# Optimization experiments

Measured on AMD Instinct MI355X. Metric: run time of the kernel, lower is better.

The kernel has to match this reference:

```python
import jax, jax.numpy as jnp
import numpy as np

WH, WW = 8, 8
NUM_HEADS = 8
DIM = 256
MLP_HIDDEN = 1024
EPS = 1e-5


def _rel_pos_index(wh, ww):
    ch, cw = np.meshgrid(np.arange(wh), np.arange(ww), indexing='ij')
    flat = np.stack([ch.ravel(), cw.ravel()])            # (2, N)
    rel = flat[:, :, None] - flat[:, None, :]            # (2, N, N)
    rel = rel.transpose(1, 2, 0).copy()                  # (N, N, 2)
    rel[:, :, 0] += wh - 1
    rel[:, :, 1] += ww - 1
    rel[:, :, 0] *= 2 * ww - 1
    return jnp.asarray(rel.sum(-1))                      # (N, N) int

REL_IDX = _rel_pos_index(WH, WW)


def _layernorm(x, g, b):
    mu = x.mean(-1, keepdims=True)
    var = ((x - mu) ** 2).mean(-1, keepdims=True)
    return (x - mu) * jax.lax.rsqrt(var + EPS) * g + b


def _window_partition(x):
    B, H, W, C = x.shape
    x = x.reshape(B, H // WH, WH, W // WW, WW, C)
    return x.transpose(0, 1, 3, 2, 4, 5).reshape(-1, WH * WW, C)


def _window_reverse(w, B, H, W):
    C = w.shape[-1]
    x = w.reshape(B, H // WH, W // WW, WH, WW, C)
    return x.transpose(0, 1, 3, 2, 4, 5).reshape(B, H, W, C)


def _window_attn(qx, kvx, qw, qb, kvw, kvb, bias_table, pw, pb):
    # qx/kvx: [Bw, N, C]; weights stored as [in, out] (torch Linear transposed)
    Bw, N, C = qx.shape
    hd = C // NUM_HEADS
    scale = hd ** -0.5
    q = (qx @ qw + qb).reshape(Bw, N, NUM_HEADS, hd).transpose(0, 2, 1, 3) * scale
    kv = (kvx @ kvw + kvb).reshape(Bw, N, 2, NUM_HEADS, hd)
    k = kv[:, :, 0].transpose(0, 2, 1, 3)
    v = kv[:, :, 1].transpose(0, 2, 1, 3)
    attn = jnp.einsum('bhnd,bhmd->bhnm', q, k)
    bias = bias_table[REL_IDX.reshape(-1)].reshape(N, N, NUM_HEADS).transpose(2, 0, 1)
    attn = jax.nn.softmax(attn + bias[None], axis=-1)
    out = jnp.einsum('bhnm,bhmd->bhnd', attn, v).transpose(0, 2, 1, 3).reshape(Bw, N, C)
    return out @ pw + pb


def setup_inputs() -> dict:
    key = jax.random.key(0)
    ks = jax.random.split(key, 16)
    B, H, W, C = 4, 160, 160, DIM
    nW = (H // WH) * (W // WW)
    N = WH * WW
    n_bias = (2 * WH - 1) * (2 * WW - 1)  # 225
    s = 0.02
    return {
        'x': jax.random.normal(ks[0], (B, H, W, C), jnp.float32),
        'enc_feat': jax.random.normal(ks[1], (B, H, W, C), jnp.float32),
        'mask_matrix': jnp.zeros((nW, N, N), jnp.float32),
        'norm1_g': jnp.ones((C,), jnp.float32),
        'norm1_b': jnp.zeros((C,), jnp.float32),
        'q1_w': jax.random.normal(ks[2], (C, C), jnp.float32) * s,
        'q1_b': jnp.zeros((C,), jnp.float32),
        'kv1_w': jax.random.normal(ks[3], (C, 2 * C), jnp.float32) * s,
        'kv1_b': jnp.zeros((2 * C,), jnp.float32),
        'bias1': jax.random.normal(ks[4], (n_bias, NUM_HEADS), jnp.float32) * s,
        'proj1_w': jax.random.normal(ks[5], (C, C), jnp.float32) * s,
        'proj1_b': jnp.zeros((C,), jnp.float32),
        'q2_w': jax.random.normal(ks[6], (C, C), jnp.float32) * s,
        'q2_b': jnp.zeros((C,), jnp.float32),
        'kv2_w': jax.random.normal(ks[7], (C, 2 * C), jnp.float32) * s,
        'kv2_b': jnp.zeros((2 * C,), jnp.float32),
        'bias2': jax.random.normal(ks[8], (n_bias, NUM_HEADS), jnp.float32) * s,
        'proj2_w': jax.random.normal(ks[9], (C, C), jnp.float32) * s,
        'proj2_b': jnp.zeros((C,), jnp.float32),
        'norm2_g': jnp.ones((C,), jnp.float32),
        'norm2_b': jnp.zeros((C,), jnp.float32),
        'fc1_w': jax.random.normal(ks[10], (C, MLP_HIDDEN), jnp.float32) * s,
        'fc1_b': jnp.zeros((MLP_HIDDEN,), jnp.float32),
        'fc2_w': jax.random.normal(ks[11], (MLP_HIDDEN, C), jnp.float32) * s,
        'fc2_b': jnp.zeros((C,), jnp.float32),
    }


def reference(x, enc_feat, mask_matrix, norm1_g, norm1_b, q1_w, q1_b, kv1_w, kv1_b,
              bias1, proj1_w, proj1_b, q2_w, q2_b, kv2_w, kv2_b, bias2, proj2_w,
              proj2_b, norm2_g, norm2_b, fc1_w, fc1_b, fc2_w, fc2_b):
    # NOTE: the source forward never passes mask_matrix into attention; faithful here.
    B, H, W, C = x.shape
    shortcut = x
    xn = _layernorm(x, norm1_g, norm1_b)
    xw = _window_partition(xn)              # [B*nW, N, C]
    ew = _window_partition(enc_feat)        # [B*nW, N, C]
    # windowed self-attention with relative position bias
    xw = _window_attn(xw, xw, q1_w, q1_b, kv1_w, kv1_b, bias1, proj1_w, proj1_b)
    # windowed cross-attention to encoder features
    xw = _window_attn(xw, ew, q2_w, q2_b, kv2_w, kv2_b, bias2, proj2_w, proj2_b)
    x = shortcut + _window_reverse(xw, B, H, W)
    h = _layernorm(x, norm2_g, norm2_b)
    h = jax.nn.gelu(h @ fc1_w + fc1_b, approximate=False) @ fc2_w + fc2_b
    return x + h
```

## Files before the change

### kernel.cpp

```cpp
#include <hip/hip_runtime.h>

typedef __attribute__((ext_vector_type(4))) float f32x4;
typedef __attribute__((ext_vector_type(8))) short bf16x8;
typedef __attribute__((ext_vector_type(8))) unsigned short ushort8;
typedef unsigned short u16;
typedef unsigned int u32;

#define LDS_AS(p) ((__attribute__((address_space(3))) void*)(p))
#define GLB_AS(p) ((const __attribute__((address_space(1))) void*)(p))

__device__ __forceinline__ u16 f2b(float f) {
    u32 u = __builtin_bit_cast(u32, f);
    u32 r = (u + 0x7fffu + ((u >> 16) & 1u)) >> 16;
    return (u16)r;
}
__device__ __forceinline__ float b2f(u16 u) {
    return __builtin_bit_cast(float, (u32)u << 16);
}

struct PrepAll {
    const float* src[8];
    u16* dst[8];
    int K[8];
    int N[8];
    float S[8];
};

__global__ __launch_bounds__(256) void prep_w(PrepAll p) {
    const int wi = blockIdx.y;
    const int K = p.K[wi], N = p.N[wi];
    for (int e = blockIdx.x * 256 + threadIdx.x; e < K * N; e += gridDim.x * 256) {
        const int k = e / N, n = e % N;
        p.dst[wi][n * K + k] = f2b(p.src[wi][e] * p.S[wi]);
    }
}

__global__ __launch_bounds__(256) void prep_bias(const float* __restrict__ t1,
                                                 const float* __restrict__ t2,
                                                 float* __restrict__ Bm) {
    const int hh = blockIdx.x;
    const int s = hh >> 3, h = hh & 7;
    const float* tab = s ? t2 : t1;
    const int j = threadIdx.x & 63;
    for (int i = threadIdx.x >> 6; i < 64; i += 4) {
        const int idx = ((i >> 3) - (j >> 3) + 7) * 15 + ((i & 7) - (j & 7) + 7);
        Bm[(long)hh * 4096 + i * 64 + j] = tab[idx * 8 + h];
    }
}

__global__ __launch_bounds__(256) void prep_bcat(const float* __restrict__ q1b,
                                                 const float* __restrict__ q2b,
                                                 float qs, float* __restrict__ q1bs,
                                                 float* __restrict__ q2bs) {
    const int g = threadIdx.x;
    q1bs[g] = qs * q1b[g];
    q2bs[g] = qs * q2b[g];
}

__global__ __launch_bounds__(256) void cast_bf(const float* __restrict__ in,
                                               u16* __restrict__ out, long n8) {
    for (long i = (long)blockIdx.x * 256 + threadIdx.x; i < n8; i += (long)gridDim.x * 256) {
        const float4 a = *(const float4*)(in + i * 8);
        const float4 b = *(const float4*)(in + i * 8 + 4);
        ushort8 o;
        o[0] = f2b(a.x); o[1] = f2b(a.y); o[2] = f2b(a.z); o[3] = f2b(a.w);
        o[4] = f2b(b.x); o[5] = f2b(b.y); o[6] = f2b(b.z); o[7] = f2b(b.w);
        *(ushort8*)(out + i * 8) = o;
    }
}

__global__ __launch_bounds__(256) void ln256(const float* __restrict__ x,
                                             const float* __restrict__ g,
                                             const float* __restrict__ b,
                                             u16* __restrict__ out) {
    const int lane = threadIdx.x & 63;
    const int c = lane * 4;
    const float4 gv = *(const float4*)(g + c);
    const float4 bv = *(const float4*)(b + c);
#pragma unroll
    for (int it = 0; it < 8; ++it) {
        const long row = (long)blockIdx.x * 32 + it * 4 + (threadIdx.x >> 6);
        const float4 v = *(const float4*)(x + row * 256 + c);
        float s = v.x + v.y + v.z + v.w;
        float s2 = v.x * v.x + v.y * v.y + v.z * v.z + v.w * v.w;
#pragma unroll
        for (int off = 32; off > 0; off >>= 1) {
            s += __shfl_xor(s, off);
            s2 += __shfl_xor(s2, off);
        }
        const float mu = s * (1.f / 256.f);
        const float rr = rsqrtf(s2 * (1.f / 256.f) - mu * mu + 1e-5f);
        ushort4 o;
        o.x = f2b((v.x - mu) * rr * gv.x + bv.x);
        o.y = f2b((v.y - mu) * rr * gv.y + bv.y);
        o.z = f2b((v.z - mu) * rr * gv.z + bv.z);
        o.w = f2b((v.w - mu) * rr * gv.w + bv.w);
        *(ushort4*)(out + row * 256 + c) = o;
    }
}

__global__ __launch_bounds__(256) void ln_add(const float* __restrict__ x,
                                              const u16* __restrict__ p,
                                              const float* __restrict__ g,
                                              const float* __restrict__ b,
                                              float* __restrict__ out,
                                              u16* __restrict__ xo) {
    const int lane = threadIdx.x & 63;
    const int c = lane * 4;
    const float4 gv = *(const float4*)(g + c);
    const float4 bv = *(const float4*)(b + c);
#pragma unroll
    for (int it = 0; it < 8; ++it) {
        const long row = (long)blockIdx.x * 32 + it * 4 + (threadIdx.x >> 6);
        float4 v = *(const float4*)(x + row * 256 + c);
        const ushort4 pb = *(const ushort4*)(p + row * 256 + c);
        v.x += b2f(pb.x); v.y += b2f(pb.y); v.z += b2f(pb.z); v.w += b2f(pb.w);
        *(float4*)(out + row * 256 + c) = v;
        float s = v.x + v.y + v.z + v.w;
        float s2 = v.x * v.x + v.y * v.y + v.z * v.z + v.w * v.w;
#pragma unroll
        for (int off = 32; off > 0; off >>= 1) {
            s += __shfl_xor(s, off);
            s2 += __shfl_xor(s2, off);
        }
        const float mu = s * (1.f / 256.f);
        const float rr = rsqrtf(s2 * (1.f / 256.f) - mu * mu + 1e-5f);
        ushort4 o;
        o.x = f2b((v.x - mu) * rr * gv.x + bv.x);
        o.y = f2b((v.y - mu) * rr * gv.y + bv.y);
        o.z = f2b((v.z - mu) * rr * gv.z + bv.z);
        o.w = f2b((v.w - mu) * rr * gv.w + bv.w);
        *(ushort4*)(xo + row * 256 + c) = o;
    }
}

template <int SAME>
__global__ __launch_bounds__(512, 1) void attn_f(const u16* __restrict__ xq,
                                                 const u16* __restrict__ xkv,
                                                 const u16* __restrict__ wq,
                                                 const u16* __restrict__ wkv,
                                                 const float* __restrict__ bq,
                                                 const float* __restrict__ bkv,
                                                 const u16* __restrict__ wp,
                                                 const float* __restrict__ bp,
                                                 const float* __restrict__ Bm,
                                                 u16* __restrict__ OUT) {
    __shared__ u16 LDS[57344];
    const int t = threadIdx.x, lane = t & 63, h = t >> 6;
    const int l15 = lane & 15, lg = lane >> 4;

    const int w = blockIdx.x;
    const int b = w / 400, rem = w % 400;
    const int wy = rem / 20, wx = rem % 20;
    const long base_t = (long)b * 25600 + wy * 1280 + wx * 8;
    auto trow = [&](int r) -> long { return base_t + (r >> 3) * 160 + (r & 7); };

#pragma unroll
    for (int j = 0; j < 4; j++) {
        const int row = j * 16 + (t >> 5);
        const int c0 = t & 31, sc = c0 ^ (row & 7);
        __builtin_amdgcn_global_load_lds(GLB_AS(xq + trow(row) * 256 + sc * 8),
                                         LDS_AS(&LDS[(j * 512 + t) * 8]), 16, 0, 0);
    }
    if (!SAME) {
#pragma unroll
        for (int j = 0; j < 4; j++) {
            const int row = j * 16 + (t >> 5);
            const int c0 = t & 31, sc = c0 ^ (row & 7);
            __builtin_amdgcn_global_load_lds(GLB_AS(xkv + trow(row) * 256 + sc * 8),
                                             LDS_AS(&LDS[16384 + (j * 512 + t) * 8]), 16, 0, 0);
        }
    }
    asm volatile("s_waitcnt vmcnt(0)" ::: "memory");
    __builtin_amdgcn_s_barrier();

    constexpr int XKV = SAME ? 0 : 16384;
    const f32x4 zz = (f32x4){0.f, 0.f, 0.f, 0.f};

    f32x4 aQ[4][2], aK[4][2], aV[4][2];
#pragma unroll
    for (int mi = 0; mi < 4; mi++)
#pragma unroll
        for (int n = 0; n < 2; n++) { aQ[mi][n] = zz; aK[mi][n] = zz; aV[mi][n] = zz; }

    const u16* wv = wkv + 256 * 256;

#define QKV_PASS(ACC, W, XB)                                                              \
    do {                                                                                  \
        bf16x8 wf[2][8];                                                                  \
        _Pragma("unroll") for (int n = 0; n < 2; n++)                                     \
            _Pragma("unroll") for (int s = 0; s < 8; s++)                                 \
                wf[n][s] = *(const bf16x8*)((W) + (h * 32 + n * 16 + l15) * 256 + s * 32 + lg * 8); \
        _Pragma("unroll") for (int s = 0; s < 8; s++) {                                   \
            bf16x8 af[4];                                                                 \
            _Pragma("unroll") for (int mi = 0; mi < 4; mi++)                              \
                af[mi] = *(const bf16x8*)&LDS[(XB) + ((mi * 16 + l15) * 32 +              \
                                              ((s * 4 + lg) ^ (l15 & 7))) * 8];           \
            _Pragma("unroll") for (int mi = 0; mi < 4; mi++)                              \
                _Pragma("unroll") for (int n = 0; n < 2; n++)                             \
                    ACC[mi][n] = __builtin_amdgcn_mfma_f32_16x16x32_bf16(af[mi], wf[n][s], ACC[mi][n], 0, 0, 0); \
        }                                                                                 \
    } while (0)

    QKV_PASS(aQ, wq, 0);
    QKV_PASS(aK, wkv, XKV);
    QKV_PASS(aV, wv, XKV);
#undef QKV_PASS
    __builtin_amdgcn_s_barrier();

    float bQ[2], bK[2], bV[2];
#pragma unroll
    for (int n = 0; n < 2; n++) {
        bQ[n] = bq[h * 32 + n * 16 + l15];
        bK[n] = bkv[h * 32 + n * 16 + l15];
        bV[n] = bkv[256 + h * 32 + n * 16 + l15];
    }

    const int S1 = h * 2560;
#pragma unroll
    for (int mi = 0; mi < 4; mi++)
#pragma unroll
        for (int n = 0; n < 2; n++)
#pragma unroll
            for (int r = 0; r < 4; r++)
                LDS[S1 + (mi * 16 + lg * 4 + r) * 40 + n * 16 + l15] = f2b(aQ[mi][n][r] + bQ[n]);
    bf16x8 qf[4];
#pragma unroll
    for (int ti = 0; ti < 4; ti++)
        qf[ti] = *(const bf16x8*)&LDS[S1 + (ti * 16 + l15) * 40 + lg * 8];
#pragma unroll
    for (int mi = 0; mi < 4; mi++)
#pragma unroll
        for (int n = 0; n < 2; n++)
#pragma unroll
            for (int r = 0; r < 4; r++)
                LDS[S1 + (mi * 16 + lg * 4 + r) * 40 + n * 16 + l15] = f2b(aK[mi][n][r] + bK[n]);
    bf16x8 kf[4];
#pragma unroll
    for (int ti = 0; ti < 4; ti++)
        kf[ti] = *(const bf16x8*)&LDS[S1 + (ti * 16 + l15) * 40 + lg * 8];

    f32x4 s4[4][4];
#pragma unroll
    for (int ti = 0; ti < 4; ti++)
#pragma unroll
        for (int tj = 0; tj < 4; tj++)
            s4[ti][tj] = __builtin_amdgcn_mfma_f32_16x16x32_bf16(qf[ti], kf[tj], zz, 0, 0, 0);

#pragma unroll
    for (int mi = 0; mi < 4; mi++)
#pragma unroll
        for (int n = 0; n < 2; n++)
#pragma unroll
            for (int r = 0; r < 4; r++)
                LDS[S1 + (n * 16 + l15) * 72 + mi * 16 + lg * 4 + r] = f2b(aV[mi][n][r] + bV[n]);

    const int PB = 20480 + h * 4608;
    const float* Bh = Bm + h * 4096;
#pragma unroll
    for (int ti = 0; ti < 4; ti++) {
#pragma unroll
        for (int r = 0; r < 4; r++) {
            const int i = ti * 16 + lg * 4 + r;
            float vv[4];
            float m = -1e30f;
#pragma unroll
            for (int tj = 0; tj < 4; tj++) {
                vv[tj] = s4[ti][tj][r] + Bh[i * 64 + tj * 16 + l15];
                m = fmaxf(m, vv[tj]);
            }
#pragma unroll
            for (int off = 1; off < 16; off <<= 1) m = fmaxf(m, __shfl_xor(m, off));
            float sum = 0.f;
#pragma unroll
            for (int tj = 0; tj < 4; tj++) {
                vv[tj] = __expf(vv[tj] - m);
                sum += vv[tj];
            }
#pragma unroll
            for (int off = 1; off < 16; off <<= 1) sum += __shfl_xor(sum, off);
            const float inv = 1.f / sum;
#pragma unroll
            for (int tj = 0; tj < 4; tj++)
                LDS[PB + i * 72 + tj * 16 + l15] = f2b(vv[tj] * inv);
        }
    }

    f32x4 o[4][2];
#pragma unroll
    for (int mi = 0; mi < 4; mi++)
#pragma unroll
        for (int n = 0; n < 2; n++) o[mi][n] = zz;
#pragma unroll
    for (int c = 0; c < 2; c++) {
        bf16x8 vf[2];
#pragma unroll
        for (int n = 0; n < 2; n++)
            vf[n] = *(const bf16x8*)&LDS[S1 + (n * 16 + l15) * 72 + c * 32 + lg * 8];
#pragma unroll
        for (int mi = 0; mi < 4; mi++) {
            bf16x8 pf = *(const bf16x8*)&LDS[PB + (mi * 16 + l15) * 72 + c * 32 + lg * 8];
#pragma unroll
            for (int n = 0; n < 2; n++)
                o[mi][n] = __builtin_amdgcn_mfma_f32_16x16x32_bf16(pf, vf[n], o[mi][n], 0, 0, 0);
        }
    }

    __builtin_amdgcn_s_barrier();
#pragma unroll
    for (int mi = 0; mi < 4; mi++)
#pragma unroll
        for (int n = 0; n < 2; n++)
#pragma unroll
            for (int r = 0; r < 4; r++)
                LDS[(mi * 16 + lg * 4 + r) * 264 + h * 32 + n * 16 + l15] = f2b(o[mi][n][r]);
    __builtin_amdgcn_s_barrier();

    bf16x8 pwf[2][8];
#pragma unroll
    for (int n = 0; n < 2; n++)
#pragma unroll
        for (int s = 0; s < 8; s++)
            pwf[n][s] = *(const bf16x8*)(wp + (h * 32 + n * 16 + l15) * 256 + s * 32 + lg * 8);
    f32x4 pacc[4][2];
#pragma unroll
    for (int mi = 0; mi < 4; mi++)
#pragma unroll
        for (int n = 0; n < 2; n++) pacc[mi][n] = zz;
#pragma unroll
    for (int s = 0; s < 8; s++) {
        bf16x8 paf[4];
#pragma unroll
        for (int mi = 0; mi < 4; mi++)
            paf[mi] = *(const bf16x8*)&LDS[(mi * 16 + l15) * 264 + s * 32 + lg * 8];
#pragma unroll
        for (int mi = 0; mi < 4; mi++)
#pragma unroll
            for (int n = 0; n < 2; n++)
                pacc[mi][n] = __builtin_amdgcn_mfma_f32_16x16x32_bf16(paf[mi], pwf[n][s], pacc[mi][n], 0, 0, 0);
    }
    float pb2[2];
#pragma unroll
    for (int n = 0; n < 2; n++) pb2[n] = bp[h * 32 + n * 16 + l15];
#pragma unroll
    for (int mi = 0; mi < 4; mi++)
#pragma unroll
        for (int n = 0; n < 2; n++)
#pragma unroll
            for (int r = 0; r < 4; r++) {
                const int i = mi * 16 + lg * 4 + r;
                OUT[trow(i) * 256 + h * 32 + n * 16 + l15] = f2b(pacc[mi][n][r] + pb2[n]);
            }
}

__global__ __launch_bounds__(512) void mlpf(const u16* __restrict__ xo,
                                            const u16* __restrict__ w1,
                                            const float* __restrict__ b1,
                                            const u16* __restrict__ w2,
                                            const float* __restrict__ b2,
                                            float* __restrict__ out) {
    __shared__ u16 W[16384];
    __shared__ u16 HS[9216];
    const int t = threadIdx.x, lane = t & 63, h = t >> 6;
    const int l15 = lane & 15, lg = lane >> 4;
    const long r0 = (long)blockIdx.x * 128 + h * 16;
    const f32x4 zz = (f32x4){0.f, 0.f, 0.f, 0.f};

    bf16x8 af[8];
#pragma unroll
    for (int s = 0; s < 8; s++)
        af[s] = *(const bf16x8*)(xo + (r0 + l15) * 256 + s * 32 + lg * 8);

    f32x4 yacc[16];
#pragma unroll
    for (int n = 0; n < 16; n++) yacc[n] = zz;

    const int hsb = h * 1152;

    for (int c = 0; c < 16; ++c) {
        if (c) __builtin_amdgcn_s_barrier();
#pragma unroll
        for (int rnd = 0; rnd < 4; rnd++) {
            const int idx = rnd * 512 + t;
            const int row = idx >> 5, c0 = idx & 31, sc = c0 ^ (row & 7);
            __builtin_amdgcn_global_load_lds(GLB_AS(w1 + (c * 64 + row) * 256 + sc * 8),
                                             LDS_AS(&W[idx * 8]), 16, 0, 0);
        }
        asm volatile("s_waitcnt vmcnt(0)" ::: "memory");
        __builtin_amdgcn_s_barrier();

        float f1bb[4];
#pragma unroll
        for (int n = 0; n < 4; n++) f1bb[n] = b1[c * 64 + n * 16 + l15];

        f32x4 hc[4];
#pragma unroll
        for (int n = 0; n < 4; n++) hc[n] = zz;
#pragma unroll
        for (int s = 0; s < 8; s++) {
            bf16x8 bf[4];
#pragma unroll
            for (int n = 0; n < 4; n++)
                bf[n] = *(const bf16x8*)&W[((n * 16 + l15) * 32 + ((s * 4 + lg) ^ (l15 & 7))) * 8];
#pragma unroll
            for (int n = 0; n < 4; n++)
                hc[n] = __builtin_amdgcn_mfma_f32_16x16x32_bf16(af[s], bf[n], hc[n], 0, 0, 0);
        }
#pragma unroll
        for (int n = 0; n < 4; n++)
#pragma unroll
            for (int r = 0; r < 4; r++) {
                float v = hc[n][r] + f1bb[n];
                v = 0.5f * v * (1.f + erff(v * 0.70710678118f));
                HS[hsb + (lg * 4 + r) * 72 + n * 16 + l15] = f2b(v);
            }
        __builtin_amdgcn_s_barrier();

#pragma unroll
        for (int rnd = 0; rnd < 4; rnd++) {
            const int idx = rnd * 512 + t;
            const int row = idx >> 3, c0 = idx & 7, sc = c0 ^ (row & 7);
            __builtin_amdgcn_global_load_lds(GLB_AS(w2 + row * 1024 + c * 64 + sc * 8),
                                             LDS_AS(&W[idx * 8]), 16, 0, 0);
        }
        asm volatile("s_waitcnt vmcnt(0)" ::: "memory");
        __builtin_amdgcn_s_barrier();

#pragma unroll
        for (int ks = 0; ks < 2; ks++) {
            bf16x8 haf = *(const bf16x8*)&HS[hsb + l15 * 72 + ks * 32 + lg * 8];
            bf16x8 bf2[16];
#pragma unroll
            for (int n = 0; n < 16; n++)
                bf2[n] = *(const bf16x8*)&W[((n * 16 + l15) * 8 + ((ks * 4 + lg) ^ (l15 & 7))) * 8];
#pragma unroll
            for (int n = 0; n < 16; n++)
                yacc[n] = __builtin_amdgcn_mfma_f32_16x16x32_bf16(haf, bf2[n], yacc[n], 0, 0, 0);
        }
    }

    float f2bb[16];
#pragma unroll
    for (int n = 0; n < 16; n++) f2bb[n] = b2[n * 16 + l15];
#pragma unroll
    for (int n = 0; n < 16; n++)
#pragma unroll
        for (int r = 0; r < 4; r++) {
            const long idx = (r0 + lg * 4 + r) * 256 + n * 16 + l15;
            out[idx] = yacc[n][r] + f2bb[n] + out[idx];
        }
}

extern "C" void kernel_launch(void* const* d_in, const int* in_sizes, int n_in,
                              void* d_out, int out_size, void* d_ws, size_t ws_size,
                              hipStream_t stream) {
    const float* x    = (const float*)d_in[0];
    const float* enc  = (const float*)d_in[1];
    const float* n1g  = (const float*)d_in[3];
    const float* n1b  = (const float*)d_in[4];
    const float* q1w  = (const float*)d_in[5];
    const float* q1b  = (const float*)d_in[6];
    const float* kv1w = (const float*)d_in[7];
    const float* kv1b = (const float*)d_in[8];
    const float* bias1 = (const float*)d_in[9];
    const float* p1w  = (const float*)d_in[10];
    const float* p1b  = (const float*)d_in[11];
    const float* q2w  = (const float*)d_in[12];
    const float* q2b  = (const float*)d_in[13];
    const float* kv2w = (const float*)d_in[14];
    const float* kv2b = (const float*)d_in[15];
    const float* bias2 = (const float*)d_in[16];
    const float* p2w  = (const float*)d_in[17];
    const float* p2bi = (const float*)d_in[18];
    const float* n2g  = (const float*)d_in[19];
    const float* n2b  = (const float*)d_in[20];
    const float* f1w  = (const float*)d_in[21];
    const float* f1b  = (const float*)d_in[22];
    const float* f2w  = (const float*)d_in[23];
    const float* f2bias = (const float*)d_in[24];
    float* out = (float*)d_out;

    char* ws = (char*)d_ws;
    size_t off = 0;
    auto alloc = [&](size_t bytes) {
        char* p = ws + off;
        off += (bytes + 255) & ~(size_t)255;
        return p;
    };
    u16* Wt    = (u16*)alloc(1048576 * 2);
    float* Bm  = (float*)alloc(16 * 4096 * 4);
    float* q1s = (float*)alloc(256 * 4);
    float* q2s = (float*)alloc(256 * 4);
    u16* xn    = (u16*)alloc(52428800);
    u16* y1    = (u16*)alloc(52428800);
    u16* pj2   = (u16*)alloc(52428800);
    u16* encb  = (u16*)alloc(52428800);

    u16 *q1t = Wt, *kv1t = Wt + 65536, *p1t = Wt + 196608, *q2t = Wt + 262144,
        *kv2t = Wt + 327680, *p2t = Wt + 458752, *f1t = Wt + 524288, *f2t = Wt + 786432;

    const float qscale = 0.17677669529663687f;

    PrepAll pa;
    pa.src[0] = q1w;  pa.dst[0] = q1t;  pa.K[0] = 256;  pa.N[0] = 256;  pa.S[0] = qscale;
    pa.src[1] = kv1w; pa.dst[1] = kv1t; pa.K[1] = 256;  pa.N[1] = 512;  pa.S[1] = 1.f;
    pa.src[2] = p1w;  pa.dst[2] = p1t;  pa.K[2] = 256;  pa.N[2] = 256;  pa.S[2] = 1.f;
    pa.src[3] = q2w;  pa.dst[3] = q2t;  pa.K[3] = 256;  pa.N[3] = 256;  pa.S[3] = qscale;
    pa.src[4] = kv2w; pa.dst[4] = kv2t; pa.K[4] = 256;  pa.N[4] = 512;  pa.S[4] = 1.f;
    pa.src[5] = p2w;  pa.dst[5] = p2t;  pa.K[5] = 256;  pa.N[5] = 256;  pa.S[5] = 1.f;
    pa.src[6] = f1w;  pa.dst[6] = f1t;  pa.K[6] = 256;  pa.N[6] = 1024; pa.S[6] = 1.f;
    pa.src[7] = f2w;  pa.dst[7] = f2t;  pa.K[7] = 1024; pa.N[7] = 256;  pa.S[7] = 1.f;
    prep_w<<<dim3(128, 8), 256, 0, stream>>>(pa);
    prep_bias<<<dim3(16), 256, 0, stream>>>(bias1, bias2, Bm);
    prep_bcat<<<dim3(1), 256, 0, stream>>>(q1b, q2b, qscale, q1s, q2s);
    cast_bf<<<dim3(2048), 256, 0, stream>>>(enc, encb, 3276800);
    ln256<<<dim3(3200), 256, 0, stream>>>(x, n1g, n1b, xn);

    attn_f<1><<<dim3(1600), 512, 0, stream>>>(xn, xn, q1t, kv1t, q1s, kv1b,
                                              p1t, p1b, Bm, y1);
    attn_f<0><<<dim3(1600), 512, 0, stream>>>(y1, encb, q2t, kv2t, q2s, kv2b,
                                              p2t, p2bi, Bm + 8 * 4096, pj2);

    ln_add<<<dim3(3200), 256, 0, stream>>>(x, pj2, n2g, n2b, out, xn);

    mlpf<<<dim3(800), 512, 0, stream>>>(xn, f1t, f1b, f2t, f2bias, out);
}
```

Before: 820.9 us.

## Shrink LDS and registers to run two blocks per CU in attention and MLP

The attention kernel shrinks its LDS footprint from about 112KB to 76KB. It does this by reusing the per-wave Q/K staging area for the probability tile and splitting the softmax-times-V step into two halves. It also loads weight fragments per k-step instead of all at once, lowering register pressure, and both kernels now request two blocks per CU. The MLP kernel loads the fc1 and fc2 weight chunks together into one larger LDS buffer, removing a barrier and load-wait phase per chunk, and uses an XOR-swizzled hidden buffer instead of padding. The risks are that two blocks per CU may not fit, and that softmax is now computed twice.

```diff
diff --git a/kernel.cpp b/kernel.cpp
--- a/kernel.cpp
+++ b/kernel.cpp
@@ -135,7 +135,7 @@
 }
 
 template <int SAME>
-__global__ __launch_bounds__(512, 1) void attn_f(const u16* __restrict__ xq,
+__global__ __launch_bounds__(512, 2) void attn_f(const u16* __restrict__ xq,
                                                  const u16* __restrict__ xkv,
                                                  const u16* __restrict__ wq,
                                                  const u16* __restrict__ wkv,
@@ -145,7 +145,7 @@
                                                  const float* __restrict__ bp,
                                                  const float* __restrict__ Bm,
                                                  u16* __restrict__ OUT) {
-    __shared__ u16 LDS[57344];
+    __shared__ u16 LDS[38912];
     const int t = threadIdx.x, lane = t & 63, h = t >> 6;
     const int l15 = lane & 15, lg = lane >> 4;
 
@@ -185,21 +185,20 @@
 
     const u16* wv = wkv + 256 * 256;
 
-#define QKV_PASS(ACC, W, XB)                                                              \
-    do {                                                                                  \
-        bf16x8 wf[2][8];                                                                  \
-        _Pragma("unroll") for (int n = 0; n < 2; n++)                                     \
-            _Pragma("unroll") for (int s = 0; s < 8; s++)                                 \
-                wf[n][s] = *(const bf16x8*)((W) + (h * 32 + n * 16 + l15) * 256 + s * 32 + lg * 8); \
-        _Pragma("unroll") for (int s = 0; s < 8; s++) {                                   \
-            bf16x8 af[4];                                                                 \
-            _Pragma("unroll") for (int mi = 0; mi < 4; mi++)                              \
-                af[mi] = *(const bf16x8*)&LDS[(XB) + ((mi * 16 + l15) * 32 +              \
-                                              ((s * 4 + lg) ^ (l15 & 7))) * 8];           \
-            _Pragma("unroll") for (int mi = 0; mi < 4; mi++)                              \
-                _Pragma("unroll") for (int n = 0; n < 2; n++)                             \
-                    ACC[mi][n] = __builtin_amdgcn_mfma_f32_16x16x32_bf16(af[mi], wf[n][s], ACC[mi][n], 0, 0, 0); \
-        }                                                                                 \
+#define QKV_PASS(ACC, W, XB)                                                               \
+    do {                                                                                   \
+        _Pragma("unroll") for (int s = 0; s < 8; s++) {                                    \
+            bf16x8 wf0 = *(const bf16x8*)((W) + (h * 32 + l15) * 256 + s * 32 + lg * 8);   \
+            bf16x8 wf1 = *(const bf16x8*)((W) + (h * 32 + 16 + l15) * 256 + s * 32 + lg * 8); \
+            bf16x8 af[4];                                                                  \
+            _Pragma("unroll") for (int mi = 0; mi < 4; mi++)                               \
+                af[mi] = *(const bf16x8*)&LDS[(XB) + ((mi * 16 + l15) * 32 +               \
+                                              ((s * 4 + lg) ^ (l15 & 7))) * 8];            \
+            _Pragma("unroll") for (int mi = 0; mi < 4; mi++) {                             \
+                ACC[mi][0] = __builtin_amdgcn_mfma_f32_16x16x32_bf16(af[mi], wf0, ACC[mi][0], 0, 0, 0); \
+                ACC[mi][1] = __builtin_amdgcn_mfma_f32_16x16x32_bf16(af[mi], wf1, ACC[mi][1], 0, 0, 0); \
+            }                                                                              \
+        }                                                                                  \
     } while (0)
 
     QKV_PASS(aQ, wq, 0);
@@ -216,29 +215,37 @@
         bV[n] = bkv[256 + h * 32 + n * 16 + l15];
     }
 
-    const int S1 = h * 2560;
+    const int SB = h * 4864;
 #pragma unroll
     for (int mi = 0; mi < 4; mi++)
 #pragma unroll
         for (int n = 0; n < 2; n++)
 #pragma unroll
             for (int r = 0; r < 4; r++)
-                LDS[S1 + (mi * 16 + lg * 4 + r) * 40 + n * 16 + l15] = f2b(aQ[mi][n][r] + bQ[n]);
+                LDS[SB + 2560 + (n * 16 + l15) * 72 + mi * 16 + lg * 4 + r] = f2b(aV[mi][n][r] + bV[n]);
+
+#pragma unroll
+    for (int mi = 0; mi < 4; mi++)
+#pragma unroll
+        for (int n = 0; n < 2; n++)
+#pragma unroll
+            for (int r = 0; r < 4; r++)
+                LDS[SB + (mi * 16 + lg * 4 + r) * 40 + n * 16 + l15] = f2b(aQ[mi][n][r] + bQ[n]);
     bf16x8 qf[4];
 #pragma unroll
     for (int ti = 0; ti < 4; ti++)
-        qf[ti] = *(const bf16x8*)&LDS[S1 + (ti * 16 + l15) * 40 + lg * 8];
+        qf[ti] = *(const bf16x8*)&LDS[SB + (ti * 16 + l15) * 40 + lg * 8];
 #pragma unroll
     for (int mi = 0; mi < 4; mi++)
 #pragma unroll
         for (int n = 0; n < 2; n++)
 #pragma unroll
             for (int r = 0; r < 4; r++)
-                LDS[S1 + (mi * 16 + lg * 4 + r) * 40 + n * 16 + l15] = f2b(aK[mi][n][r] + bK[n]);
+                LDS[SB + (mi * 16 + lg * 4 + r) * 40 + n * 16 + l15] = f2b(aK[mi][n][r] + bK[n]);
     bf16x8 kf[4];
 #pragma unroll
     for (int ti = 0; ti < 4; ti++)
-        kf[ti] = *(const bf16x8*)&LDS[S1 + (ti * 16 + l15) * 40 + lg * 8];
+        kf[ti] = *(const bf16x8*)&LDS[SB + (ti * 16 + l15) * 40 + lg * 8];
 
     f32x4 s4[4][4];
 #pragma unroll
@@ -247,59 +254,50 @@
         for (int tj = 0; tj < 4; tj++)
             s4[ti][tj] = __builtin_amdgcn_mfma_f32_16x16x32_bf16(qf[ti], kf[tj], zz, 0, 0, 0);
 
-#pragma unroll
-    for (int mi = 0; mi < 4; mi++)
+    const float* Bh = Bm + h * 4096;
+    f32x4 o[4][2];
+#pragma unroll
+    for (int mi = 0; mi < 4; mi++)
+#pragma unroll
+        for (int n = 0; n < 2; n++) o[mi][n] = zz;
+
+#pragma unroll
+    for (int hf = 0; hf < 2; ++hf) {
+#pragma unroll
+        for (int ti = 0; ti < 4; ti++) {
+#pragma unroll
+            for (int r = 0; r < 4; r++) {
+                const int i = ti * 16 + lg * 4 + r;
+                float vv[4];
+                float m = -1e30f;
+#pragma unroll
+                for (int tj = 0; tj < 4; tj++) {
+                    vv[tj] = s4[ti][tj][r] + Bh[i * 64 + tj * 16 + l15];
+                    m = fmaxf(m, vv[tj]);
+                }
+#pragma unroll
+                for (int off = 1; off < 16; off <<= 1) m = fmaxf(m, __shfl_xor(m, off));
+                float sum = 0.f;
+#pragma unroll
+                for (int tj = 0; tj < 4; tj++) {
+                    vv[tj] = __expf(vv[tj] - m);
+                    sum += vv[tj];
+                }
+#pragma unroll
+                for (int off = 1; off < 16; off <<= 1) sum += __shfl_xor(sum, off);
+                const float inv = 1.f / sum;
+#pragma unroll
+                for (int u = 0; u < 2; u++)
+                    LDS[SB + i * 40 + u * 16 + l15] = f2b(vv[hf * 2 + u] * inv);
+            }
+        }
+        bf16x8 vf[2];
 #pragma unroll
         for (int n = 0; n < 2; n++)
-#pragma unroll
-            for (int r = 0; r < 4; r++)
-                LDS[S1 + (n * 16 + l15) * 72 + mi * 16 + lg * 4 + r] = f2b(aV[mi][n][r] + bV[n]);
-
-    const int PB = 20480 + h * 4608;
-    const float* Bh = Bm + h * 4096;
-#pragma unroll
-    for (int ti = 0; ti < 4; ti++) {
-#pragma unroll
-        for (int r = 0; r < 4; r++) {
-            const int i = ti * 16 + lg * 4 + r;
-            float vv[4];
-            float m = -1e30f;
-#pragma unroll
-            for (int tj = 0; tj < 4; tj++) {
-                vv[tj] = s4[ti][tj][r] + Bh[i * 64 + tj * 16 + l15];
-                m = fmaxf(m, vv[tj]);
-            }
-#pragma unroll
-            for (int off = 1; off < 16; off <<= 1) m = fmaxf(m, __shfl_xor(m, off));
-            float sum = 0.f;
-#pragma unroll
-            for (int tj = 0; tj < 4; tj++) {
-                vv[tj] = __expf(vv[tj] - m);
-                sum += vv[tj];
-            }
-#pragma unroll
-            for (int off = 1; off < 16; off <<= 1) sum += __shfl_xor(sum, off);
-            const float inv = 1.f / sum;
-#pragma unroll
-            for (int tj = 0; tj < 4; tj++)
-                LDS[PB + i * 72 + tj * 16 + l15] = f2b(vv[tj] * inv);
-        }
-    }
-
-    f32x4 o[4][2];
-#pragma unroll
-    for (int mi = 0; mi < 4; mi++)
-#pragma unroll
-        for (int n = 0; n < 2; n++) o[mi][n] = zz;
-#pragma unroll
-    for (int c = 0; c < 2; c++) {
-        bf16x8 vf[2];
-#pragma unroll
-        for (int n = 0; n < 2; n++)
-            vf[n] = *(const bf16x8*)&LDS[S1 + (n * 16 + l15) * 72 + c * 32 + lg * 8];
+            vf[n] = *(const bf16x8*)&LDS[SB + 2560 + (n * 16 + l15) * 72 + hf * 32 + lg * 8];
 #pragma unroll
         for (int mi = 0; mi < 4; mi++) {
-            bf16x8 pf = *(const bf16x8*)&LDS[PB + (mi * 16 + l15) * 72 + c * 32 + lg * 8];
+            bf16x8 pf = *(const bf16x8*)&LDS[SB + (mi * 16 + l15) * 40 + lg * 8];
 #pragma unroll
             for (int n = 0; n < 2; n++)
                 o[mi][n] = __builtin_amdgcn_mfma_f32_16x16x32_bf16(pf, vf[n], o[mi][n], 0, 0, 0);
@@ -353,14 +351,14 @@
             }
 }
 
-__global__ __launch_bounds__(512) void mlpf(const u16* __restrict__ xo,
-                                            const u16* __restrict__ w1,
-                                            const float* __restrict__ b1,
-                                            const u16* __restrict__ w2,
-                                            const float* __restrict__ b2,
-                                            float* __restrict__ out) {
-    __shared__ u16 W[16384];
-    __shared__ u16 HS[9216];
+__global__ __launch_bounds__(512, 2) void mlpf(const u16* __restrict__ xo,
+                                               const u16* __restrict__ w1,
+                                               const float* __restrict__ b1,
+                                               const u16* __restrict__ w2,
+                                               const float* __restrict__ b2,
+                                               float* __restrict__ out) {
+    __shared__ u16 W[32768];
+    __shared__ u16 HS[8192];
     const int t = threadIdx.x, lane = t & 63, h = t >> 6;
     const int l15 = lane & 15, lg = lane >> 4;
     const long r0 = (long)blockIdx.x * 128 + h * 16;
@@ -375,16 +373,23 @@
 #pragma unroll
     for (int n = 0; n < 16; n++) yacc[n] = zz;
 
-    const int hsb = h * 1152;
+    const int hsb = h * 1024;
 
     for (int c = 0; c < 16; ++c) {
         if (c) __builtin_amdgcn_s_barrier();
 #pragma unroll
         for (int rnd = 0; rnd < 4; rnd++) {
-            const int idx = rnd * 512 + t;
-            const int row = idx >> 5, c0 = idx & 31, sc = c0 ^ (row & 7);
-            __builtin_amdgcn_global_load_lds(GLB_AS(w1 + (c * 64 + row) * 256 + sc * 8),
-                                             LDS_AS(&W[idx * 8]), 16, 0, 0);
+            const int ia = rnd * 512 + t;
+            const int rowa = ia >> 5, sca = (ia & 31) ^ (rowa & 7);
+            __builtin_amdgcn_global_load_lds(GLB_AS(w1 + (c * 64 + rowa) * 256 + sca * 8),
+                                             LDS_AS(&W[ia * 8]), 16, 0, 0);
+        }
+#pragma unroll
+        for (int rnd = 0; rnd < 4; rnd++) {
+            const int ib = rnd * 512 + t;
+            const int rowb = ib >> 3, scb = (ib & 7) ^ (rowb & 7);
+            __builtin_amdgcn_global_load_lds(GLB_AS(w2 + rowb * 1024 + c * 64 + scb * 8),
+                                             LDS_AS(&W[16384 + ib * 8]), 16, 0, 0);
         }
         asm volatile("s_waitcnt vmcnt(0)" ::: "memory");
         __builtin_amdgcn_s_barrier();
@@ -412,27 +417,17 @@
             for (int r = 0; r < 4; r++) {
                 float v = hc[n][r] + f1bb[n];
                 v = 0.5f * v * (1.f + erff(v * 0.70710678118f));
-                HS[hsb + (lg * 4 + r) * 72 + n * 16 + l15] = f2b(v);
+                const int row = lg * 4 + r;
+                HS[hsb + row * 64 + ((n * 16 + l15) ^ ((row & 7) << 3))] = f2b(v);
             }
-        __builtin_amdgcn_s_barrier();
-
-#pragma unroll
-        for (int rnd = 0; rnd < 4; rnd++) {
-            const int idx = rnd * 512 + t;
-            const int row = idx >> 3, c0 = idx & 7, sc = c0 ^ (row & 7);
-            __builtin_amdgcn_global_load_lds(GLB_AS(w2 + row * 1024 + c * 64 + sc * 8),
-                                             LDS_AS(&W[idx * 8]), 16, 0, 0);
-        }
-        asm volatile("s_waitcnt vmcnt(0)" ::: "memory");
-        __builtin_amdgcn_s_barrier();
 
 #pragma unroll
         for (int ks = 0; ks < 2; ks++) {
-            bf16x8 haf = *(const bf16x8*)&HS[hsb + l15 * 72 + ks * 32 + lg * 8];
+            bf16x8 haf = *(const bf16x8*)&HS[hsb + l15 * 64 + ((ks * 32 + lg * 8) ^ ((l15 & 7) << 3))];
             bf16x8 bf2[16];
 #pragma unroll
             for (int n = 0; n < 16; n++)
-                bf2[n] = *(const bf16x8*)&W[((n * 16 + l15) * 8 + ((ks * 4 + lg) ^ (l15 & 7))) * 8];
+                bf2[n] = *(const bf16x8*)&W[16384 + ((n * 16 + l15) * 8 + ((ks * 4 + lg) ^ (l15 & 7))) * 8];
 #pragma unroll
             for (int n = 0; n < 16; n++)
                 yacc[n] = __builtin_amdgcn_mfma_f32_16x16x32_bf16(haf, bf2[n], yacc[n], 0, 0, 0);
```

After: 902.2 us. 9.9% more time.
